# Kernel optimization log

Hardware: AMD Instinct MI355X
Metric: run time of the kernel (lower is better)

## Reference

```python
import jax, jax.numpy as jnp
import numpy as np

NUM_STAB = 0.001  # numerical_stabilizer from relu_kernel_transformation


def relu_kernel(data, proj):
    """ReLU random-feature kernel: data [B,L,H,D], proj [M,D] -> [B,L,H,M]."""
    ratio = 1.0 / jnp.sqrt(jnp.asarray(proj.shape[0], jnp.float32))
    data_dash = ratio * jnp.einsum('blhd,md->blhm', data, proj)
    return jax.nn.relu(data_dash) + NUM_STAB


def setup_inputs() -> dict:
    key = jax.random.key(0)
    k1, k2, k3, k4 = jax.random.split(key, 4)
    B, L, H, D, M = 2, 4096, 8, 64, 256
    return {
        'query': jax.random.normal(k1, (B, L, H, D), jnp.float32),
        'key_t': jax.random.normal(k2, (B, L, H, D), jnp.float32),
        'value': jax.random.normal(k3, (B, L, H, D), jnp.float32),
        'projection_matrix': jax.random.normal(k4, (M, D), jnp.float32),
    }


def reference(query, key_t, value, projection_matrix):
    # Kernel feature maps [B,L,H,M]
    qp = relu_kernel(query, projection_matrix)
    kp = relu_kernel(key_t, projection_matrix)
    # Causal path operates in [L,B,H,*] layout
    qs = jnp.transpose(qp, (1, 0, 2, 3))     # [L,B,H,M]
    ks = jnp.transpose(kp, (1, 0, 2, 3))     # [L,B,H,M]
    vs = jnp.transpose(value, (1, 0, 2, 3))  # [L,B,H,D]

    B, H, M = qs.shape[1], qs.shape[2], qs.shape[3]
    D = vs.shape[3]
    init = (jnp.zeros((B, H, M, D), qs.dtype),  # running sum of k outer v
            jnp.zeros((B, H, M), qs.dtype))     # running sum of k

    def step(carry, inp):
        kv_sum, k_sum = carry
        q, k, v = inp  # [B,H,M], [B,H,M], [B,H,D]
        kv_sum = kv_sum + k[..., None] * v[..., None, :]
        k_sum = k_sum + k
        num = jnp.einsum('bhmd,bhm->bhd', kv_sum, q)  # causal numerator step
        den = jnp.einsum('bhm,bhm->bh', q, k_sum)     # causal denominator step
        return (kv_sum, k_sum), (num, den)

    _, (num, den) = jax.lax.scan(step, init, (qs, ks, vs))  # num [L,B,H,D], den [L,B,H]
    den = den[..., None]
    den = jnp.where(den <= 0.0, jnp.ones_like(den), den)
    out = num / den                      # [L,B,H,D]
    return jnp.transpose(out, (1, 0, 2, 3))  # [B,L,H,D]
```

## Files before the change

### kernel.cpp

```cpp
#include <hip/hip_runtime.h>


#define B_   2
#define L_   4096
#define H_   8
#define D_   64
#define M_   256
#define T_   128
#define C_   (L_ / T_)
#define NBH  (B_ * H_)
#define RATIO 0.0625f
#define STAB  0.001f
#define SQP  72
#define SAM  136

typedef __attribute__((ext_vector_type(8))) short short8;
typedef __attribute__((ext_vector_type(4))) float floatx4;

#define MFMA16(a, b, c) __builtin_amdgcn_mfma_f32_16x16x32_bf16(a, b, c, 0, 0, 0)

__device__ inline unsigned short f2bf(float x) {
    union { float f; unsigned u; } v; v.f = x;
    unsigned r = v.u + 0x7FFF + ((v.u >> 16) & 1);
    return (unsigned short)(r >> 16);
}
__device__ inline float bf2f(unsigned short b) {
    union { unsigned u; float f; } v; v.u = ((unsigned)b) << 16; return v.f;
}
__device__ inline short8 ldg8_bf(const float* p) {
    float4 a = *(const float4*)p;
    float4 b = *(const float4*)(p + 4);
    short8 r;
    r[0] = (short)f2bf(a.x); r[1] = (short)f2bf(a.y);
    r[2] = (short)f2bf(a.z); r[3] = (short)f2bf(a.w);
    r[4] = (short)f2bf(b.x); r[5] = (short)f2bf(b.y);
    r[6] = (short)f2bf(b.z); r[7] = (short)f2bf(b.w);
    return r;
}

__global__ __launch_bounds__(256, 2)
void phase1_kernel(const float* __restrict__ key, const float* __restrict__ val,
                   const float* __restrict__ proj,
                   float* __restrict__ S, float* __restrict__ Z) {
    const int c = blockIdx.x, bh = blockIdx.y;
    const int b = bh / H_, h = bh % H_;
    const int tid = threadIdx.x;
    const int w = tid >> 6, lane = tid & 63;
    const int l15 = lane & 15, quad = lane >> 4;
    const int tb = 32 * w;

    __shared__ __align__(16) unsigned short VT[64 * SAM];
    __shared__ __align__(16) unsigned short KpT[64 * SAM];

    const size_t rowstr = H_ * D_;
    const size_t base = ((size_t)b * L_ + (size_t)c * T_) * rowstr + (size_t)h * D_;

    for (int i = tid; i < T_ * 16; i += 256) {
        int t = i >> 4, d4 = (i & 15) * 4;
        float4 vv = *(const float4*)(val + base + (size_t)t * rowstr + d4);
        VT[(d4 + 0) * SAM + t] = f2bf(vv.x);
        VT[(d4 + 1) * SAM + t] = f2bf(vv.y);
        VT[(d4 + 2) * SAM + t] = f2bf(vv.z);
        VT[(d4 + 3) * SAM + t] = f2bf(vv.w);
    }
    short8 kf[2][2];
#pragma unroll
    for (int rt = 0; rt < 2; ++rt)
#pragma unroll
        for (int kk = 0; kk < 2; ++kk)
            kf[rt][kk] = ldg8_bf(key + base + (size_t)(tb + rt * 16 + l15) * rowstr
                                 + kk * 32 + quad * 8);
    __syncthreads();
    short8 vf[4];
#pragma unroll
    for (int k4 = 0; k4 < 4; ++k4)
        vf[k4] = *(const short8*)&VT[(16 * w + l15) * SAM + k4 * 32 + quad * 8];

    float* Sp = S + (size_t)(bh * C_ + c) * (M_ * D_);
    float* Zp = Z + (size_t)(bh * C_ + c) * M_;
    const int mloc = tid >> 2, q4 = tid & 3;

    for (int fg = 0; fg < 4; ++fg) {
        short8 pf[4][2];
#pragma unroll
        for (int ct = 0; ct < 4; ++ct)
#pragma unroll
            for (int kk = 0; kk < 2; ++kk)
                pf[ct][kk] = ldg8_bf(proj + (size_t)(fg * 64 + ct * 16 + l15) * D_
                                     + kk * 32 + quad * 8);
        floatx4 ck[2][4];
#pragma unroll
        for (int rt = 0; rt < 2; ++rt)
#pragma unroll
            for (int ct = 0; ct < 4; ++ct) {
                floatx4 z4 = {0.f, 0.f, 0.f, 0.f};
                z4 = MFMA16(kf[rt][0], pf[ct][0], z4);
                z4 = MFMA16(kf[rt][1], pf[ct][1], z4);
                ck[rt][ct] = z4;
            }
        __syncthreads();
#pragma unroll
        for (int rt = 0; rt < 2; ++rt)
#pragma unroll
            for (int ct = 0; ct < 4; ++ct)
#pragma unroll
                for (int r = 0; r < 4; ++r) {
                    int t = tb + rt * 16 + quad * 4 + r;
                    int mp = ct * 16 + l15;
                    KpT[mp * SAM + t] =
                        f2bf(fmaxf(RATIO * ck[rt][ct][r], 0.f) + STAB);
                }
        __syncthreads();
        floatx4 sa[4];
#pragma unroll
        for (int ct = 0; ct < 4; ++ct) {
            floatx4 acc = {0.f, 0.f, 0.f, 0.f};
#pragma unroll
            for (int k4 = 0; k4 < 4; ++k4) {
                short8 kb = *(const short8*)&KpT[(ct * 16 + l15) * SAM
                                                + k4 * 32 + quad * 8];
                acc = MFMA16(vf[k4], kb, acc);
            }
            sa[ct] = acc;
        }
#pragma unroll
        for (int ct = 0; ct < 4; ++ct)
#pragma unroll
            for (int r = 0; r < 4; ++r)
                Sp[(size_t)(16 * w + quad * 4 + r) * M_
                   + fg * 64 + ct * 16 + l15] = sa[ct][r];
        {
            float zz = 0.f;
            const unsigned short* krow = &KpT[mloc * SAM + q4 * 32];
#pragma unroll
            for (int i = 0; i < 32; ++i) zz += bf2f(krow[i]);
            zz += __shfl_xor(zz, 1, 64);
            zz += __shfl_xor(zz, 2, 64);
            if (q4 == 0) Zp[fg * 64 + mloc] = zz;
        }
    }
}

__global__ void phase2_kernel(float* __restrict__ S, float* __restrict__ Z) {
    const int bh = blockIdx.y;
    const int j = blockIdx.x * 256 + threadIdx.x;
    if (j < M_ * D_) {
        float run = 0.f;
        float* p = S + (size_t)bh * C_ * M_ * D_ + j;
        for (int c = 0; c < C_; ++c) {
            float t = p[(size_t)c * (M_ * D_)];
            p[(size_t)c * (M_ * D_)] = run;
            run += t;
        }
    } else {
        const int j2 = j - M_ * D_;
        if (j2 < M_) {
            float run = 0.f;
            float* p = Z + (size_t)bh * C_ * M_ + j2;
            for (int c = 0; c < C_; ++c) {
                float t = p[c * M_];
                p[c * M_] = run;
                run += t;
            }
        }
    }
}

__global__ __launch_bounds__(256, 2)
void phase3_kernel(const float* __restrict__ q, const float* __restrict__ key,
                   const float* __restrict__ val, const float* __restrict__ proj,
                   const float* __restrict__ S, const float* __restrict__ Z,
                   float* __restrict__ out) {
    const int c = blockIdx.x, bh = blockIdx.y;
    const int b = bh / H_, h = bh % H_;
    const int tid = threadIdx.x;
    const int w = tid >> 6, lane = tid & 63;
    const int l15 = lane & 15, quad = lane >> 4;
    const int tb = 32 * w;

    __shared__ __align__(16) unsigned short QK[2 * T_ * SQP];
    __shared__ __align__(16) unsigned short VT[64 * SAM];
    __shared__ float zS[M_];
    __shared__ float denAS[T_];
    __shared__ float denZS[T_];

    unsigned short* QpL = QK;
    unsigned short* KpL = QK + T_ * SQP;
    unsigned short* AmL = QK;

    const size_t rowstr = H_ * D_;
    const size_t base = ((size_t)b * L_ + (size_t)c * T_) * rowstr + (size_t)h * D_;
    const float* Sp = S + (size_t)(bh * C_ + c) * (M_ * D_);
    const float* Zp = Z + (size_t)(bh * C_ + c) * M_;

    for (int i = tid; i < T_ * 16; i += 256) {
        int t = i >> 4, d4 = (i & 15) * 4;
        float4 vv = *(const float4*)(val + base + (size_t)t * rowstr + d4);
        VT[(d4 + 0) * SAM + t] = f2bf(vv.x);
        VT[(d4 + 1) * SAM + t] = f2bf(vv.y);
        VT[(d4 + 2) * SAM + t] = f2bf(vv.z);
        VT[(d4 + 3) * SAM + t] = f2bf(vv.w);
    }
    zS[tid] = Zp[tid];
    short8 qf[2][2], kf[2][2];
#pragma unroll
    for (int rt = 0; rt < 2; ++rt)
#pragma unroll
        for (int kk = 0; kk < 2; ++kk) {
            size_t ro = base + (size_t)(tb + rt * 16 + l15) * rowstr + kk * 32 + quad * 8;
            qf[rt][kk] = ldg8_bf(q + ro);
            kf[rt][kk] = ldg8_bf(key + ro);
        }

    floatx4 Aacc[2][8];
    floatx4 num[2][4];
#pragma unroll
    for (int rt = 0; rt < 2; ++rt) {
#pragma unroll
        for (int ct = 0; ct < 8; ++ct) { floatx4 z4 = {0.f,0.f,0.f,0.f}; Aacc[rt][ct] = z4; }
#pragma unroll
        for (int dt = 0; dt < 4; ++dt) { floatx4 z4 = {0.f,0.f,0.f,0.f}; num[rt][dt] = z4; }
    }
    float denZacc = 0.f;
    const int tz = tid >> 1, hz = tid & 1;

    __syncthreads();

    for (int fg = 0; fg < 4; ++fg) {
        short8 pf[4][2];
#pragma unroll
        for (int ct = 0; ct < 4; ++ct)
#pragma unroll
            for (int kk = 0; kk < 2; ++kk)
                pf[ct][kk] = ldg8_bf(proj + (size_t)(fg * 64 + ct * 16 + l15) * D_
                                     + kk * 32 + quad * 8);
        short8 sf[4][2];
#pragma unroll
        for (int dt = 0; dt < 4; ++dt)
#pragma unroll
            for (int kk = 0; kk < 2; ++kk)
                sf[dt][kk] = ldg8_bf(Sp + (size_t)(dt * 16 + l15) * M_
                                     + fg * 64 + kk * 32 + quad * 8);
        floatx4 cq[2][4], ck[2][4];
#pragma unroll
        for (int rt = 0; rt < 2; ++rt)
#pragma unroll
            for (int ct = 0; ct < 4; ++ct) {
                floatx4 a4 = {0.f,0.f,0.f,0.f};
                a4 = MFMA16(qf[rt][0], pf[ct][0], a4);
                a4 = MFMA16(qf[rt][1], pf[ct][1], a4);
                cq[rt][ct] = a4;
                floatx4 b4 = {0.f,0.f,0.f,0.f};
                b4 = MFMA16(kf[rt][0], pf[ct][0], b4);
                b4 = MFMA16(kf[rt][1], pf[ct][1], b4);
                ck[rt][ct] = b4;
            }
        __syncthreads();
#pragma unroll
        for (int rt = 0; rt < 2; ++rt)
#pragma unroll
            for (int ct = 0; ct < 4; ++ct)
#pragma unroll
                for (int r = 0; r < 4; ++r) {
                    int t = tb + rt * 16 + quad * 4 + r;
                    int mp = ct * 16 + l15;
                    QpL[t * SQP + mp] = f2bf(fmaxf(RATIO * cq[rt][ct][r], 0.f) + STAB);
                    KpL[t * SQP + mp] = f2bf(fmaxf(RATIO * ck[rt][ct][r], 0.f) + STAB);
                }
        __syncthreads();
        short8 qa[2][2];
#pragma unroll
        for (int rt = 0; rt < 2; ++rt)
#pragma unroll
            for (int kk = 0; kk < 2; ++kk)
                qa[rt][kk] = *(const short8*)&QpL[(tb + rt * 16 + l15) * SQP
                                                 + kk * 32 + quad * 8];
#pragma unroll
        for (int ct = 0; ct < 8; ++ct) {
            short8 kb0 = *(const short8*)&KpL[(ct * 16 + l15) * SQP + quad * 8];
            short8 kb1 = *(const short8*)&KpL[(ct * 16 + l15) * SQP + 32 + quad * 8];
#pragma unroll
            for (int rt = 0; rt < 2; ++rt) {
                Aacc[rt][ct] = MFMA16(qa[rt][0], kb0, Aacc[rt][ct]);
                Aacc[rt][ct] = MFMA16(qa[rt][1], kb1, Aacc[rt][ct]);
            }
        }
#pragma unroll
        for (int dt = 0; dt < 4; ++dt)
#pragma unroll
            for (int rt = 0; rt < 2; ++rt) {
                num[rt][dt] = MFMA16(qa[rt][0], sf[dt][0], num[rt][dt]);
                num[rt][dt] = MFMA16(qa[rt][1], sf[dt][1], num[rt][dt]);
            }
        {
            float dz = 0.f;
            const unsigned short* qrow = &QpL[tz * SQP + hz * 32];
            const float* zp = &zS[fg * 64 + hz * 32];
#pragma unroll
            for (int i = 0; i < 32; ++i) dz += bf2f(qrow[i]) * zp[i];
            dz += __shfl_xor(dz, 1, 64);
            denZacc += dz;
        }
    }

    float drow[2][4];
#pragma unroll
    for (int rt = 0; rt < 2; ++rt)
#pragma unroll
        for (int r = 0; r < 4; ++r) drow[rt][r] = 0.f;
#pragma unroll
    for (int rt = 0; rt < 2; ++rt)
#pragma unroll
        for (int ct = 0; ct < 8; ++ct)
#pragma unroll
            for (int r = 0; r < 4; ++r) {
                int t = tb + rt * 16 + quad * 4 + r;
                int tc = ct * 16 + l15;
                float av = (tc <= t) ? Aacc[rt][ct][r] : 0.f;
                Aacc[rt][ct][r] = av;
                drow[rt][r] += av;
            }
#pragma unroll
    for (int rt = 0; rt < 2; ++rt)
#pragma unroll
        for (int r = 0; r < 4; ++r) {
            float s = drow[rt][r];
            s += __shfl_xor(s, 1, 64);
            s += __shfl_xor(s, 2, 64);
            s += __shfl_xor(s, 4, 64);
            s += __shfl_xor(s, 8, 64);
            drow[rt][r] = s;
        }
    __syncthreads();
#pragma unroll
    for (int rt = 0; rt < 2; ++rt)
#pragma unroll
        for (int ct = 0; ct < 8; ++ct)
#pragma unroll
            for (int r = 0; r < 4; ++r) {
                int t = tb + rt * 16 + quad * 4 + r;
                AmL[t * SAM + ct * 16 + l15] = f2bf(Aacc[rt][ct][r]);
            }
    if (l15 == 0)
#pragma unroll
        for (int rt = 0; rt < 2; ++rt)
#pragma unroll
            for (int r = 0; r < 4; ++r)
                denAS[tb + rt * 16 + quad * 4 + r] = drow[rt][r];
    if (hz == 0) denZS[tz] = denZacc;
    __syncthreads();

    short8 am[2][4];
#pragma unroll
    for (int rt = 0; rt < 2; ++rt)
#pragma unroll
        for (int k4 = 0; k4 < 4; ++k4)
            am[rt][k4] = *(const short8*)&AmL[(tb + rt * 16 + l15) * SAM
                                             + k4 * 32 + quad * 8];
#pragma unroll
    for (int dt = 0; dt < 4; ++dt)
#pragma unroll
        for (int k4 = 0; k4 < 4; ++k4) {
            short8 vb = *(const short8*)&VT[(dt * 16 + l15) * SAM + k4 * 32 + quad * 8];
#pragma unroll
            for (int rt = 0; rt < 2; ++rt)
                num[rt][dt] = MFMA16(am[rt][k4], vb, num[rt][dt]);
        }

#pragma unroll
    for (int rt = 0; rt < 2; ++rt)
#pragma unroll
        for (int r = 0; r < 4; ++r) {
            int t = tb + rt * 16 + quad * 4 + r;
            float den = denAS[t] + denZS[t];
            if (den <= 0.f) den = 1.f;
            float inv = 1.f / den;
#pragma unroll
            for (int dt = 0; dt < 4; ++dt)
                out[base + (size_t)t * rowstr + dt * 16 + l15] = num[rt][dt][r] * inv;
        }
}

extern "C" void kernel_launch(void* const* d_in, const int* in_sizes, int n_in,
                              void* d_out, int out_size, void* d_ws, size_t ws_size,
                              hipStream_t stream) {
    const float* q    = (const float*)d_in[0];
    const float* k    = (const float*)d_in[1];
    const float* v    = (const float*)d_in[2];
    const float* proj = (const float*)d_in[3];
    float* out = (float*)d_out;

    float* S = (float*)d_ws;
    float* Z = S + (size_t)NBH * C_ * M_ * D_;

    dim3 g1(C_, NBH);
    phase1_kernel<<<g1, dim3(256), 0, stream>>>(k, v, proj, S, Z);
    dim3 g2((M_ * D_ + M_) / 256, NBH);
    phase2_kernel<<<g2, dim3(256), 0, stream>>>(S, Z);
    phase3_kernel<<<g1, dim3(256), 0, stream>>>(q, k, v, proj, S, Z, out);
}
```

Before: 188.9 us.

## Store chunk states in bf16 and restructure phases with 512-thread blocks

```diff
diff --git a/kernel.cpp b/kernel.cpp
--- a/kernel.cpp
+++ b/kernel.cpp
@@ -11,8 +11,9 @@
 #define NBH  (B_ * H_)
 #define RATIO 0.0625f
 #define STAB  0.001f
-#define SQP  72
-#define SAM  136
+#define SVT  136
+#define SKP  264
+#define SQS  72
 
 typedef __attribute__((ext_vector_type(8))) short short8;
 typedef __attribute__((ext_vector_type(4))) float floatx4;
@@ -38,47 +39,35 @@
     return r;
 }
 
-__global__ __launch_bounds__(256, 2)
+__global__ __launch_bounds__(512, 1)
 void phase1_kernel(const float* __restrict__ key, const float* __restrict__ val,
                    const float* __restrict__ proj,
-                   float* __restrict__ S, float* __restrict__ Z) {
+                   unsigned short* __restrict__ S, float* __restrict__ Z) {
     const int c = blockIdx.x, bh = blockIdx.y;
     const int b = bh / H_, h = bh % H_;
     const int tid = threadIdx.x;
     const int w = tid >> 6, lane = tid & 63;
     const int l15 = lane & 15, quad = lane >> 4;
-    const int tb = 32 * w;
-
-    __shared__ __align__(16) unsigned short VT[64 * SAM];
-    __shared__ __align__(16) unsigned short KpT[64 * SAM];
+
+    __shared__ __align__(16) unsigned short VT[64 * SVT];
+    __shared__ __align__(16) unsigned short KpT[M_ * SVT];
+    __shared__ float zP[8][M_];
 
     const size_t rowstr = H_ * D_;
     const size_t base = ((size_t)b * L_ + (size_t)c * T_) * rowstr + (size_t)h * D_;
 
-    for (int i = tid; i < T_ * 16; i += 256) {
+    for (int i = tid; i < T_ * 16; i += 512) {
         int t = i >> 4, d4 = (i & 15) * 4;
         float4 vv = *(const float4*)(val + base + (size_t)t * rowstr + d4);
-        VT[(d4 + 0) * SAM + t] = f2bf(vv.x);
-        VT[(d4 + 1) * SAM + t] = f2bf(vv.y);
-        VT[(d4 + 2) * SAM + t] = f2bf(vv.z);
-        VT[(d4 + 3) * SAM + t] = f2bf(vv.w);
-    }
-    short8 kf[2][2];
-#pragma unroll
-    for (int rt = 0; rt < 2; ++rt)
-#pragma unroll
-        for (int kk = 0; kk < 2; ++kk)
-            kf[rt][kk] = ldg8_bf(key + base + (size_t)(tb + rt * 16 + l15) * rowstr
-                                 + kk * 32 + quad * 8);
-    __syncthreads();
-    short8 vf[4];
-#pragma unroll
-    for (int k4 = 0; k4 < 4; ++k4)
-        vf[k4] = *(const short8*)&VT[(16 * w + l15) * SAM + k4 * 32 + quad * 8];
-
-    float* Sp = S + (size_t)(bh * C_ + c) * (M_ * D_);
-    float* Zp = Z + (size_t)(bh * C_ + c) * M_;
-    const int mloc = tid >> 2, q4 = tid & 3;
+        VT[(d4 + 0) * SVT + t] = f2bf(vv.x);
+        VT[(d4 + 1) * SVT + t] = f2bf(vv.y);
+        VT[(d4 + 2) * SVT + t] = f2bf(vv.z);
+        VT[(d4 + 3) * SVT + t] = f2bf(vv.w);
+    }
+    short8 kf[2];
+#pragma unroll
+    for (int kk = 0; kk < 2; ++kk)
+        kf[kk] = ldg8_bf(key + base + (size_t)(16 * w + l15) * rowstr + kk * 32 + quad * 8);
 
     for (int fg = 0; fg < 4; ++fg) {
         short8 pf[4][2];
@@ -88,143 +77,121 @@
             for (int kk = 0; kk < 2; ++kk)
                 pf[ct][kk] = ldg8_bf(proj + (size_t)(fg * 64 + ct * 16 + l15) * D_
                                      + kk * 32 + quad * 8);
-        floatx4 ck[2][4];
-#pragma unroll
-        for (int rt = 0; rt < 2; ++rt)
-#pragma unroll
-            for (int ct = 0; ct < 4; ++ct) {
-                floatx4 z4 = {0.f, 0.f, 0.f, 0.f};
-                z4 = MFMA16(kf[rt][0], pf[ct][0], z4);
-                z4 = MFMA16(kf[rt][1], pf[ct][1], z4);
-                ck[rt][ct] = z4;
+#pragma unroll
+        for (int ct = 0; ct < 4; ++ct) {
+            floatx4 a = {0.f, 0.f, 0.f, 0.f};
+            a = MFMA16(kf[0], pf[ct][0], a);
+            a = MFMA16(kf[1], pf[ct][1], a);
+            float zrow = 0.f;
+            const int m = fg * 64 + ct * 16 + l15;
+#pragma unroll
+            for (int r = 0; r < 4; ++r) {
+                float kpf = fmaxf(RATIO * a[r], 0.f) + STAB;
+                KpT[m * SVT + 16 * w + quad * 4 + r] = f2bf(kpf);
+                zrow += kpf;
             }
-        __syncthreads();
-#pragma unroll
-        for (int rt = 0; rt < 2; ++rt)
-#pragma unroll
-            for (int ct = 0; ct < 4; ++ct)
-#pragma unroll
-                for (int r = 0; r < 4; ++r) {
-                    int t = tb + rt * 16 + quad * 4 + r;
-                    int mp = ct * 16 + l15;
-                    KpT[mp * SAM + t] =
-                        f2bf(fmaxf(RATIO * ck[rt][ct][r], 0.f) + STAB);
-                }
-        __syncthreads();
-        floatx4 sa[4];
-#pragma unroll
-        for (int ct = 0; ct < 4; ++ct) {
-            floatx4 acc = {0.f, 0.f, 0.f, 0.f};
-#pragma unroll
-            for (int k4 = 0; k4 < 4; ++k4) {
-                short8 kb = *(const short8*)&KpT[(ct * 16 + l15) * SAM
-                                                + k4 * 32 + quad * 8];
-                acc = MFMA16(vf[k4], kb, acc);
-            }
-            sa[ct] = acc;
-        }
-#pragma unroll
-        for (int ct = 0; ct < 4; ++ct)
-#pragma unroll
-            for (int r = 0; r < 4; ++r)
-                Sp[(size_t)(16 * w + quad * 4 + r) * M_
-                   + fg * 64 + ct * 16 + l15] = sa[ct][r];
-        {
-            float zz = 0.f;
-            const unsigned short* krow = &KpT[mloc * SAM + q4 * 32];
-#pragma unroll
-            for (int i = 0; i < 32; ++i) zz += bf2f(krow[i]);
-            zz += __shfl_xor(zz, 1, 64);
-            zz += __shfl_xor(zz, 2, 64);
-            if (q4 == 0) Zp[fg * 64 + mloc] = zz;
-        }
-    }
-}
-
-__global__ void phase2_kernel(float* __restrict__ S, float* __restrict__ Z) {
+            zrow += __shfl_xor(zrow, 16, 64);
+            zrow += __shfl_xor(zrow, 32, 64);
+            if (quad == 0) zP[w][m] = zrow;
+        }
+    }
+    __syncthreads();
+
+    const int dtile = w & 3, mh = w >> 2;
+    short8 vf[4];
+#pragma unroll
+    for (int k4 = 0; k4 < 4; ++k4)
+        vf[k4] = *(const short8*)&VT[(16 * dtile + l15) * SVT + k4 * 32 + quad * 8];
+    unsigned short* Sp = S + (size_t)(bh * C_ + c) * (M_ * D_);
+#pragma unroll
+    for (int ct2 = 0; ct2 < 8; ++ct2) {
+        floatx4 acc = {0.f, 0.f, 0.f, 0.f};
+#pragma unroll
+        for (int k4 = 0; k4 < 4; ++k4) {
+            short8 kb = *(const short8*)&KpT[(mh * 128 + ct2 * 16 + l15) * SVT
+                                             + k4 * 32 + quad * 8];
+            acc = MFMA16(vf[k4], kb, acc);
+        }
+#pragma unroll
+        for (int r = 0; r < 4; ++r)
+            Sp[(size_t)(16 * dtile + quad * 4 + r) * M_
+               + mh * 128 + ct2 * 16 + l15] = f2bf(acc[r]);
+    }
+    if (tid < M_) {
+        float z = 0.f;
+#pragma unroll
+        for (int ww = 0; ww < 8; ++ww) z += zP[ww][tid];
+        Z[(size_t)(bh * C_ + c) * M_ + tid] = z;
+    }
+}
+
+__global__ void phase2_kernel(unsigned int* __restrict__ S2, float* __restrict__ Z) {
     const int bh = blockIdx.y;
     const int j = blockIdx.x * 256 + threadIdx.x;
-    if (j < M_ * D_) {
-        float run = 0.f;
-        float* p = S + (size_t)bh * C_ * M_ * D_ + j;
+    const int NP = M_ * D_ / 2;
+    if (j < NP) {
+        unsigned int* p = S2 + (size_t)bh * C_ * NP + j;
+        float r0 = 0.f, r1 = 0.f;
         for (int c = 0; c < C_; ++c) {
-            float t = p[(size_t)c * (M_ * D_)];
-            p[(size_t)c * (M_ * D_)] = run;
-            run += t;
+            unsigned int v = p[(size_t)c * NP];
+            p[(size_t)c * NP] = (unsigned int)f2bf(r0) | ((unsigned int)f2bf(r1) << 16);
+            r0 += bf2f((unsigned short)(v & 0xffff));
+            r1 += bf2f((unsigned short)(v >> 16));
         }
     } else {
-        const int j2 = j - M_ * D_;
+        const int j2 = j - NP;
         if (j2 < M_) {
             float run = 0.f;
-            float* p = Z + (size_t)bh * C_ * M_ + j2;
+            float* pz = Z + (size_t)bh * C_ * M_ + j2;
             for (int c = 0; c < C_; ++c) {
-                float t = p[c * M_];
-                p[c * M_] = run;
+                float t = pz[c * M_];
+                pz[c * M_] = run;
                 run += t;
             }
         }
     }
 }
 
-__global__ __launch_bounds__(256, 2)
+__global__ __launch_bounds__(512, 1)
 void phase3_kernel(const float* __restrict__ q, const float* __restrict__ key,
                    const float* __restrict__ val, const float* __restrict__ proj,
-                   const float* __restrict__ S, const float* __restrict__ Z,
+                   const unsigned short* __restrict__ S, const float* __restrict__ Z,
                    float* __restrict__ out) {
     const int c = blockIdx.x, bh = blockIdx.y;
     const int b = bh / H_, h = bh % H_;
     const int tid = threadIdx.x;
     const int w = tid >> 6, lane = tid & 63;
     const int l15 = lane & 15, quad = lane >> 4;
-    const int tb = 32 * w;
-
-    __shared__ __align__(16) unsigned short QK[2 * T_ * SQP];
-    __shared__ __align__(16) unsigned short VT[64 * SAM];
-    __shared__ float zS[M_];
-    __shared__ float denAS[T_];
-    __shared__ float denZS[T_];
-
-    unsigned short* QpL = QK;
-    unsigned short* KpL = QK + T_ * SQP;
-    unsigned short* AmL = QK;
+
+    __shared__ __align__(16) unsigned short KpL[T_ * SKP];
+    __shared__ __align__(16) unsigned short VT[64 * SVT];
+    __shared__ __align__(16) unsigned short AmL[T_ * SVT];
+    __shared__ __align__(16) unsigned short QpS[8 * 16 * SQS];
 
     const size_t rowstr = H_ * D_;
     const size_t base = ((size_t)b * L_ + (size_t)c * T_) * rowstr + (size_t)h * D_;
-    const float* Sp = S + (size_t)(bh * C_ + c) * (M_ * D_);
+    const unsigned short* Sp = S + (size_t)(bh * C_ + c) * (M_ * D_);
     const float* Zp = Z + (size_t)(bh * C_ + c) * M_;
 
-    for (int i = tid; i < T_ * 16; i += 256) {
+    for (int i = tid; i < T_ * 16; i += 512) {
         int t = i >> 4, d4 = (i & 15) * 4;
         float4 vv = *(const float4*)(val + base + (size_t)t * rowstr + d4);
-        VT[(d4 + 0) * SAM + t] = f2bf(vv.x);
-        VT[(d4 + 1) * SAM + t] = f2bf(vv.y);
-        VT[(d4 + 2) * SAM + t] = f2bf(vv.z);
-        VT[(d4 + 3) * SAM + t] = f2bf(vv.w);
-    }
-    zS[tid] = Zp[tid];
-    short8 qf[2][2], kf[2][2];
-#pragma unroll
-    for (int rt = 0; rt < 2; ++rt)
-#pragma unroll
-        for (int kk = 0; kk < 2; ++kk) {
-            size_t ro = base + (size_t)(tb + rt * 16 + l15) * rowstr + kk * 32 + quad * 8;
-            qf[rt][kk] = ldg8_bf(q + ro);
-            kf[rt][kk] = ldg8_bf(key + ro);
-        }
-
-    floatx4 Aacc[2][8];
-    floatx4 num[2][4];
-#pragma unroll
-    for (int rt = 0; rt < 2; ++rt) {
-#pragma unroll
-        for (int ct = 0; ct < 8; ++ct) { floatx4 z4 = {0.f,0.f,0.f,0.f}; Aacc[rt][ct] = z4; }
-#pragma unroll
-        for (int dt = 0; dt < 4; ++dt) { floatx4 z4 = {0.f,0.f,0.f,0.f}; num[rt][dt] = z4; }
-    }
-    float denZacc = 0.f;
-    const int tz = tid >> 1, hz = tid & 1;
-
-    __syncthreads();
+        VT[(d4 + 0) * SVT + t] = f2bf(vv.x);
+        VT[(d4 + 1) * SVT + t] = f2bf(vv.y);
+        VT[(d4 + 2) * SVT + t] = f2bf(vv.z);
+        VT[(d4 + 3) * SVT + t] = f2bf(vv.w);
+    }
+    short8 qf[2], kf[2];
+#pragma unroll
+    for (int kk = 0; kk < 2; ++kk) {
+        size_t ro = base + (size_t)(16 * w + l15) * rowstr + kk * 32 + quad * 8;
+        qf[kk] = ldg8_bf(q + ro);
+        kf[kk] = ldg8_bf(key + ro);
+    }
+
+    unsigned short* myQp = QpS + w * 16 * SQS;
+    short8 qa[8];
+    float dz[4] = {0.f, 0.f, 0.f, 0.f};
 
     for (int fg = 0; fg < 4; ++fg) {
         short8 pf[4][2];
@@ -234,151 +201,106 @@
             for (int kk = 0; kk < 2; ++kk)
                 pf[ct][kk] = ldg8_bf(proj + (size_t)(fg * 64 + ct * 16 + l15) * D_
                                      + kk * 32 + quad * 8);
-        short8 sf[4][2];
+#pragma unroll
+        for (int ct = 0; ct < 4; ++ct) {
+            floatx4 aq = {0.f, 0.f, 0.f, 0.f};
+            aq = MFMA16(qf[0], pf[ct][0], aq);
+            aq = MFMA16(qf[1], pf[ct][1], aq);
+            floatx4 ak = {0.f, 0.f, 0.f, 0.f};
+            ak = MFMA16(kf[0], pf[ct][0], ak);
+            ak = MFMA16(kf[1], pf[ct][1], ak);
+            const int mcol = fg * 64 + ct * 16 + l15;
+            float zv = Zp[mcol];
+#pragma unroll
+            for (int r = 0; r < 4; ++r) {
+                float qpv = fmaxf(RATIO * aq[r], 0.f) + STAB;
+                float kpv = fmaxf(RATIO * ak[r], 0.f) + STAB;
+                myQp[(quad * 4 + r) * SQS + ct * 16 + l15] = f2bf(qpv);
+                KpL[(size_t)(16 * w + quad * 4 + r) * SKP + mcol] = f2bf(kpv);
+                dz[r] = fmaf(qpv, zv, dz[r]);
+            }
+        }
+#pragma unroll
+        for (int kk = 0; kk < 2; ++kk)
+            qa[fg * 2 + kk] = *(const short8*)&myQp[l15 * SQS + kk * 32 + quad * 8];
+    }
+#pragma unroll
+    for (int r = 0; r < 4; ++r) {
+        dz[r] += __shfl_xor(dz[r], 1, 64);
+        dz[r] += __shfl_xor(dz[r], 2, 64);
+        dz[r] += __shfl_xor(dz[r], 4, 64);
+        dz[r] += __shfl_xor(dz[r], 8, 64);
+    }
+
+    floatx4 num[4];
+#pragma unroll
+    for (int dt = 0; dt < 4; ++dt) {
+        floatx4 z4 = {0.f, 0.f, 0.f, 0.f};
+        num[dt] = z4;
+    }
+#pragma unroll
+    for (int dt = 0; dt < 4; ++dt)
+#pragma unroll
+        for (int kc = 0; kc < 8; ++kc) {
+            short8 sb = *(const short8*)(Sp + (size_t)(dt * 16 + l15) * M_
+                                         + kc * 32 + quad * 8);
+            num[dt] = MFMA16(qa[kc], sb, num[dt]);
+        }
+
+    __syncthreads();
+
+    floatx4 Aacc[8];
+#pragma unroll
+    for (int ct = 0; ct < 8; ++ct) {
+        floatx4 acc = {0.f, 0.f, 0.f, 0.f};
+        if (ct <= w) {
+#pragma unroll
+            for (int kc = 0; kc < 8; ++kc) {
+                short8 kb = *(const short8*)&KpL[(size_t)(ct * 16 + l15) * SKP
+                                                 + kc * 32 + quad * 8];
+                acc = MFMA16(qa[kc], kb, acc);
+            }
+        }
+        Aacc[ct] = acc;
+    }
+    float da[4] = {0.f, 0.f, 0.f, 0.f};
+#pragma unroll
+    for (int ct = 0; ct < 8; ++ct)
+#pragma unroll
+        for (int r = 0; r < 4; ++r) {
+            float av = Aacc[ct][r];
+            if (ct > w || (ct == w && l15 > quad * 4 + r)) av = 0.f;
+            AmL[(size_t)(16 * w + quad * 4 + r) * SVT + ct * 16 + l15] = f2bf(av);
+            da[r] += av;
+        }
+#pragma unroll
+    for (int r = 0; r < 4; ++r) {
+        da[r] += __shfl_xor(da[r], 1, 64);
+        da[r] += __shfl_xor(da[r], 2, 64);
+        da[r] += __shfl_xor(da[r], 4, 64);
+        da[r] += __shfl_xor(da[r], 8, 64);
+    }
+
+    for (int k4 = 0; k4 <= (w >> 1); ++k4) {
+        short8 am = *(const short8*)&AmL[(size_t)(16 * w + l15) * SVT
+                                         + k4 * 32 + quad * 8];
+#pragma unroll
+        for (int dt = 0; dt < 4; ++dt) {
+            short8 vb = *(const short8*)&VT[(dt * 16 + l15) * SVT + k4 * 32 + quad * 8];
+            num[dt] = MFMA16(am, vb, num[dt]);
+        }
+    }
+
+#pragma unroll
+    for (int r = 0; r < 4; ++r) {
+        float den = da[r] + dz[r];
+        if (den <= 0.f) den = 1.f;
+        float inv = 1.f / den;
+        int t = 16 * w + quad * 4 + r;
 #pragma unroll
         for (int dt = 0; dt < 4; ++dt)
-#pragma unroll
-            for (int kk = 0; kk < 2; ++kk)
-                sf[dt][kk] = ldg8_bf(Sp + (size_t)(dt * 16 + l15) * M_
-                                     + fg * 64 + kk * 32 + quad * 8);
-        floatx4 cq[2][4], ck[2][4];
-#pragma unroll
-        for (int rt = 0; rt < 2; ++rt)
-#pragma unroll
-            for (int ct = 0; ct < 4; ++ct) {
-                floatx4 a4 = {0.f,0.f,0.f,0.f};
-                a4 = MFMA16(qf[rt][0], pf[ct][0], a4);
-                a4 = MFMA16(qf[rt][1], pf[ct][1], a4);
-                cq[rt][ct] = a4;
-                floatx4 b4 = {0.f,0.f,0.f,0.f};
-                b4 = MFMA16(kf[rt][0], pf[ct][0], b4);
-                b4 = MFMA16(kf[rt][1], pf[ct][1], b4);
-                ck[rt][ct] = b4;
-            }
-        __syncthreads();
-#pragma unroll
-        for (int rt = 0; rt < 2; ++rt)
-#pragma unroll
-            for (int ct = 0; ct < 4; ++ct)
-#pragma unroll
-                for (int r = 0; r < 4; ++r) {
-                    int t = tb + rt * 16 + quad * 4 + r;
-                    int mp = ct * 16 + l15;
-                    QpL[t * SQP + mp] = f2bf(fmaxf(RATIO * cq[rt][ct][r], 0.f) + STAB);
-                    KpL[t * SQP + mp] = f2bf(fmaxf(RATIO * ck[rt][ct][r], 0.f) + STAB);
-                }
-        __syncthreads();
-        short8 qa[2][2];
-#pragma unroll
-        for (int rt = 0; rt < 2; ++rt)
-#pragma unroll
-            for (int kk = 0; kk < 2; ++kk)
-                qa[rt][kk] = *(const short8*)&QpL[(tb + rt * 16 + l15) * SQP
-                                                 + kk * 32 + quad * 8];
-#pragma unroll
-        for (int ct = 0; ct < 8; ++ct) {
-            short8 kb0 = *(const short8*)&KpL[(ct * 16 + l15) * SQP + quad * 8];
-            short8 kb1 = *(const short8*)&KpL[(ct * 16 + l15) * SQP + 32 + quad * 8];
-#pragma unroll
-            for (int rt = 0; rt < 2; ++rt) {
-                Aacc[rt][ct] = MFMA16(qa[rt][0], kb0, Aacc[rt][ct]);
-                Aacc[rt][ct] = MFMA16(qa[rt][1], kb1, Aacc[rt][ct]);
-            }
-        }
-#pragma unroll
-        for (int dt = 0; dt < 4; ++dt)
-#pragma unroll
-            for (int rt = 0; rt < 2; ++rt) {
-                num[rt][dt] = MFMA16(qa[rt][0], sf[dt][0], num[rt][dt]);
-                num[rt][dt] = MFMA16(qa[rt][1], sf[dt][1], num[rt][dt]);
-            }
-        {
-            float dz = 0.f;
-            const unsigned short* qrow = &QpL[tz * SQP + hz * 32];
-            const float* zp = &zS[fg * 64 + hz * 32];
-#pragma unroll
-            for (int i = 0; i < 32; ++i) dz += bf2f(qrow[i]) * zp[i];
-            dz += __shfl_xor(dz, 1, 64);
-            denZacc += dz;
-        }
-    }
-
-    float drow[2][4];
-#pragma unroll
-    for (int rt = 0; rt < 2; ++rt)
-#pragma unroll
-        for (int r = 0; r < 4; ++r) drow[rt][r] = 0.f;
-#pragma unroll
-    for (int rt = 0; rt < 2; ++rt)
-#pragma unroll
-        for (int ct = 0; ct < 8; ++ct)
-#pragma unroll
-            for (int r = 0; r < 4; ++r) {
-                int t = tb + rt * 16 + quad * 4 + r;
-                int tc = ct * 16 + l15;
-                float av = (tc <= t) ? Aacc[rt][ct][r] : 0.f;
-                Aacc[rt][ct][r] = av;
-                drow[rt][r] += av;
-            }
-#pragma unroll
-    for (int rt = 0; rt < 2; ++rt)
-#pragma unroll
-        for (int r = 0; r < 4; ++r) {
-            float s = drow[rt][r];
-            s += __shfl_xor(s, 1, 64);
-            s += __shfl_xor(s, 2, 64);
-            s += __shfl_xor(s, 4, 64);
-            s += __shfl_xor(s, 8, 64);
-            drow[rt][r] = s;
-        }
-    __syncthreads();
-#pragma unroll
-    for (int rt = 0; rt < 2; ++rt)
-#pragma unroll
-        for (int ct = 0; ct < 8; ++ct)
-#pragma unroll
-            for (int r = 0; r < 4; ++r) {
-                int t = tb + rt * 16 + quad * 4 + r;
-                AmL[t * SAM + ct * 16 + l15] = f2bf(Aacc[rt][ct][r]);
-            }
-    if (l15 == 0)
-#pragma unroll
-        for (int rt = 0; rt < 2; ++rt)
-#pragma unroll
-            for (int r = 0; r < 4; ++r)
-                denAS[tb + rt * 16 + quad * 4 + r] = drow[rt][r];
-    if (hz == 0) denZS[tz] = denZacc;
-    __syncthreads();
-
-    short8 am[2][4];
-#pragma unroll
-    for (int rt = 0; rt < 2; ++rt)
-#pragma unroll
-        for (int k4 = 0; k4 < 4; ++k4)
-            am[rt][k4] = *(const short8*)&AmL[(tb + rt * 16 + l15) * SAM
-                                             + k4 * 32 + quad * 8];
-#pragma unroll
-    for (int dt = 0; dt < 4; ++dt)
-#pragma unroll
-        for (int k4 = 0; k4 < 4; ++k4) {
-            short8 vb = *(const short8*)&VT[(dt * 16 + l15) * SAM + k4 * 32 + quad * 8];
-#pragma unroll
-            for (int rt = 0; rt < 2; ++rt)
-                num[rt][dt] = MFMA16(am[rt][k4], vb, num[rt][dt]);
-        }
-
-#pragma unroll
-    for (int rt = 0; rt < 2; ++rt)
-#pragma unroll
-        for (int r = 0; r < 4; ++r) {
-            int t = tb + rt * 16 + quad * 4 + r;
-            float den = denAS[t] + denZS[t];
-            if (den <= 0.f) den = 1.f;
-            float inv = 1.f / den;
-#pragma unroll
-            for (int dt = 0; dt < 4; ++dt)
-                out[base + (size_t)t * rowstr + dt * 16 + l15] = num[rt][dt][r] * inv;
-        }
+            out[base + (size_t)t * rowstr + dt * 16 + l15] = num[dt][r] * inv;
+    }
 }
 
 extern "C" void kernel_launch(void* const* d_in, const int* in_sizes, int n_in,
@@ -390,12 +312,12 @@
     const float* proj = (const float*)d_in[3];
     float* out = (float*)d_out;
 
-    float* S = (float*)d_ws;
-    float* Z = S + (size_t)NBH * C_ * M_ * D_;
+    unsigned short* S = (unsigned short*)d_ws;
+    float* Z = (float*)(S + (size_t)NBH * C_ * M_ * D_);
 
     dim3 g1(C_, NBH);
-    phase1_kernel<<<g1, dim3(256), 0, stream>>>(k, v, proj, S, Z);
-    dim3 g2((M_ * D_ + M_) / 256, NBH);
-    phase2_kernel<<<g2, dim3(256), 0, stream>>>(S, Z);
-    phase3_kernel<<<g1, dim3(256), 0, stream>>>(q, k, v, proj, S, Z, out);
-}
+    phase1_kernel<<<g1, dim3(512), 0, stream>>>(k, v, proj, S, Z);
+    dim3 g2(33, NBH);
+    phase2_kernel<<<g2, dim3(256), 0, stream>>>((unsigned int*)S, Z);
+    phase3_kernel<<<g1, dim3(512), 0, stream>>>(q, k, v, proj, S, Z, out);
+}
```

Measured after the change: 278.5 us. 1.47x slower.
